# Kernel tuning notes

Hardware: AMD Instinct MI355X
Metric: run time of the kernel (lower is better)

The kernel has to match this reference:

```python
import jax, jax.numpy as jnp
import numpy as np

N, E, H, D, F_IN = 50000, 400000, 2, 128, 5
EPS = 1e-5  # BatchNorm eps

def _bn(x, gamma, beta, rm, rv):
    # eval-mode BatchNorm1d using running stats
    return (x - rm) * jax.lax.rsqrt(rv + EPS) * gamma + beta

def setup_inputs() -> dict:
    key = jax.random.key(0)
    ks = jax.random.split(key, 24)
    r = lambda i, shape, s=1.0: jax.random.normal(ks[i], shape, jnp.float32) * s
    u = lambda i, shape: jax.random.uniform(ks[i], shape, jnp.float32)
    return {
        "h": r(0, (N, F_IN)),
        "edge_index": jax.random.randint(ks[1], (2, E), 0, N),
        "edge_weight": r(2, (E, 1)),
        # BatchNorm1d(5)
        "gamma1": 1.0 + r(3, (F_IN,), 0.1), "beta1": r(4, (F_IN,), 0.1),
        "rm1": r(5, (F_IN,), 0.1), "rv1": 0.5 + u(6, (F_IN,)),
        # GATv2Conv params (lin_l, lin_r with bias; lin_edge no bias; att; out bias)
        "Wl": r(7, (F_IN, H * D), 0.2), "bl": r(8, (H * D,), 0.1),
        "Wr": r(9, (F_IN, H * D), 0.2), "br": r(10, (H * D,), 0.1),
        "We": r(11, (1, H * D), 0.2),
        "att": r(12, (H, D), 0.2),
        "bias_gat": r(13, (D,), 0.1),
        # fc1 + BatchNorm1d(128)
        "W1": r(14, (D, D), 0.08), "b1": r(15, (D,), 0.1),
        "gamma2": 1.0 + r(16, (D,), 0.1), "beta2": r(17, (D,), 0.1),
        "rm2": r(18, (D,), 0.1), "rv2": 0.5 + u(19, (D,)),
        # fc2
        "W2": r(20, (D, F_IN), 0.08), "b2": r(21, (F_IN,), 0.1),
    }

def reference(h, edge_index, edge_weight, gamma1, beta1, rm1, rv1,
              Wl, bl, Wr, br, We, att, bias_gat,
              W1, b1, gamma2, beta2, rm2, rv2, W2, b2):
    src, dst = edge_index[0], edge_index[1]
    h = _bn(h, gamma1, beta1, rm1, rv1)
    xl = (h @ Wl + bl).reshape(N, H, D)   # source transform (messages)
    xr = (h @ Wr + br).reshape(N, H, D)   # destination transform
    e = (edge_weight @ We).reshape(E, H, D)
    # GATv2: score = att . leaky_relu(x_j + x_i + edge_emb), slope 0.2
    z = jax.nn.leaky_relu(xl[src] + xr[dst] + e, 0.2)          # [E,H,D]
    logits = jnp.einsum('ehd,hd->eh', z, att)                   # [E,H]
    # segment softmax over edges sharing a destination node
    mx = jax.ops.segment_max(logits, dst, num_segments=N)       # [N,H]
    ex = jnp.exp(logits - mx[dst])
    den = jax.ops.segment_sum(ex, dst, num_segments=N)
    alpha = ex / (den[dst] + 1e-16)                             # [E,H]
    msg = xl[src] * alpha[:, :, None]                           # [E,H,D]
    ssum = jax.ops.segment_sum(msg, dst, num_segments=N)        # [N,H,D]
    cnt = jax.ops.segment_sum(jnp.ones((E,), jnp.float32), dst, num_segments=N)
    out = ssum / jnp.maximum(cnt, 1.0)[:, None, None]           # aggr='mean'
    out = out.mean(axis=1) + bias_gat                           # concat=False -> head mean
    out = out @ W1 + b1
    out = _bn(out, gamma2, beta2, rm2, rv2)
    out = jax.nn.leaky_relu(out, 0.01)
    # dropout is identity in eval mode
    out = out @ W2 + b2                                         # [N,5]
    return out
```

## Files before the change

kernel.cpp:

```cpp
#include <hip/hip_runtime.h>

#define N_NODES 50000
#define N_EDGES 400000
#define F_INP 5
#define HD 256
#define BN_EPS 1e-5f

typedef short v8s __attribute__((ext_vector_type(8)));
typedef float v4f __attribute__((ext_vector_type(4)));
typedef unsigned v4u __attribute__((ext_vector_type(4)));

#define OFF_HBN  0
#define OFF_ACC  400000
#define OFF_BPK  1200000
#define OFF_WF   1202048
#define OFF_W2P  1204096

__device__ __forceinline__ unsigned short f2bf(float f) {
    unsigned u = __float_as_uint(f);
    return (unsigned short)((u + 0x7FFFu + ((u >> 16) & 1u)) >> 16);
}
__device__ __forceinline__ unsigned pk2(float a, float b) {
    return (unsigned)f2bf(a) | ((unsigned)f2bf(b) << 16);
}

__device__ __forceinline__ float wcat(int k, int c, const float* Wl, const float* Wr,
                                      const float* We, const float* bl, const float* br) {
    if (k < 5)   return Wl[k * HD + c];
    if (k < 10)  return Wr[(k - 5) * HD + c];
    if (k == 10) return We[c];
    return bl[c] + br[c];
}

__global__ void k_prep(const float* __restrict__ h, const float* __restrict__ g1,
                       const float* __restrict__ be1, const float* __restrict__ rm1,
                       const float* __restrict__ rv1,
                       const float* __restrict__ Wl, const float* __restrict__ bl,
                       const float* __restrict__ Wr, const float* __restrict__ br,
                       const float* __restrict__ We, const float* __restrict__ att,
                       float* __restrict__ hbn8, float* __restrict__ acc,
                       unsigned* __restrict__ Bpk) {
    int i = blockIdx.x * blockDim.x + threadIdx.x;
    if (i < N_NODES * 16) acc[i] = 0.f;
    if (i < N_NODES * 8) {
        int f = i & 7, n = i >> 3;
        float v = 0.f;
        if (f < F_INP) {
            float x = h[n * F_INP + f];
            v = (x - rm1[f]) * rsqrtf(rv1[f] + BN_EPS) * g1[f] + be1[f];
        }
        hbn8[i] = v;
    }
    if (i < 1024) {
        int t = i >> 6, l = i & 63;
        int g = l >> 4, c = t * 16 + (l & 15);
        unsigned d0 = 0, d1 = 0;
        if (g < 3) {
            int kb = 4 * g;
            d0 = pk2(wcat(kb + 0, c, Wl, Wr, We, bl, br),
                     wcat(kb + 1, c, Wl, Wr, We, bl, br));
            d1 = pk2(wcat(kb + 2, c, Wl, Wr, We, bl, br),
                     wcat(kb + 3, c, Wl, Wr, We, bl, br));
        }
        Bpk[(t * 64 + l) * 2 + 0] = d0;
        Bpk[(t * 64 + l) * 2 + 1] = d1;
    }
}

__global__ void k_pack2(const float* __restrict__ Wl, const float* __restrict__ bl,
                        const float* __restrict__ bias_gat,
                        const float* __restrict__ W1, const float* __restrict__ b1,
                        const float* __restrict__ g2, const float* __restrict__ be2,
                        const float* __restrict__ rm2, const float* __restrict__ rv2,
                        const float* __restrict__ W2,
                        float* __restrict__ Wf, float* __restrict__ W2p) {
    int k = blockIdx.x;
    int c = threadIdx.x;
    const float* base = (k == 0) ? bl
                      : (k == 1) ? bl + 128
                      : (k < 7)  ? Wl + (k - 2) * HD
                      : (k < 12) ? Wl + (k - 7) * HD + 128
                                 : bias_gat;
    float sum = 0.f;
#pragma unroll 8
    for (int d = 0; d < 128; ++d) sum += base[d] * W1[d * 128 + c];
    if (k == 12) sum += b1[c];
    Wf[c * 16 + k] = sum;
    if (k == 0) {
        float sc = g2[c] * rsqrtf(rv2[c] + BN_EPS);
        Wf[c * 16 + 13] = sc;
        Wf[c * 16 + 14] = be2[c] - rm2[c] * sc;
        Wf[c * 16 + 15] = 0.f;
#pragma unroll
        for (int f = 0; f < 8; ++f)
            W2p[c * 8 + f] = (f < 5) ? W2[c * 5 + f] : 0.f;
    }
}

__launch_bounds__(256)
__global__ void k_edge(const float* __restrict__ hbn8, const int* __restrict__ ei,
                       const float* __restrict__ ew, const unsigned* __restrict__ Bpk,
                       const float* __restrict__ att, float* __restrict__ acc) {
    int lane = threadIdx.x & 63;
    int wv = threadIdx.x >> 6;
    int g = lane >> 4, e16 = lane & 15;

    v8s B[16];
    float AT[16];
#pragma unroll
    for (int t = 0; t < 16; ++t) {
        unsigned d0 = Bpk[(t * 64 + lane) * 2 + 0];
        unsigned d1 = Bpk[(t * 64 + lane) * 2 + 1];
        v4u u = {d0, d1, 0u, 0u};
        B[t] = __builtin_bit_cast(v8s, u);
        AT[t] = att[t * 16 + e16];
    }

    int wid = blockIdx.x * 4 + wv;
    int nw = gridDim.x * 4;
    const int NT = N_EDGES / 16;

    int q13 = lane / 13;
    int j13 = lane - q13 * 13;
    bool sc_act = lane < 52;
    int kk = (j13 < 6) ? j13 - 1 : j13 - 7;
    int kc = min(max(kk, 0), 4);

    float x0 = 0, x1 = 0, x2 = 0, x3 = 0, x4 = 0,
          x5 = 0, x6 = 0, x7 = 0, x8 = 0, x9 = 0, x10 = 0;
    int dst_reg = 0;
    if (wid < NT && lane < 16) {
        int e = wid * 16 + lane;
        int src = ei[e];
        dst_reg = ei[N_EDGES + e];
        x10 = ew[e];
        float4 s4 = *(const float4*)&hbn8[src * 8];
        x0 = s4.x; x1 = s4.y; x2 = s4.z; x3 = s4.w;
        x4 = hbn8[src * 8 + 4];
        float4 d4 = *(const float4*)&hbn8[dst_reg * 8];
        x5 = d4.x; x6 = d4.y; x7 = d4.z; x8 = d4.w;
        x9 = hbn8[dst_reg * 8 + 4];
    }

    for (int tile = wid; tile < NT; tile += nw) {
        float b0 = __shfl(x0, e16), b1 = __shfl(x1, e16), b2 = __shfl(x2, e16),
              b3 = __shfl(x3, e16), b4 = __shfl(x4, e16), b5 = __shfl(x5, e16),
              b6 = __shfl(x6, e16), b7 = __shfl(x7, e16), b8 = __shfl(x8, e16),
              b9 = __shfl(x9, e16), b10 = __shfl(x10, e16);
        int dst_b = __shfl(dst_reg, e16);

        float a0 = (g == 0) ? b0 : (g == 1) ? b4 : b8;
        float a1 = (g == 0) ? b1 : (g == 1) ? b5 : b9;
        float a2 = (g == 0) ? b2 : (g == 1) ? b6 : b10;
        float a3 = (g == 0) ? b3 : (g == 1) ? b7 : 1.0f;
        unsigned ua0 = (g < 3) ? pk2(a0, a1) : 0u;
        unsigned ua1 = (g < 3) ? pk2(a2, a3) : 0u;
        v4u uav = {ua0, ua1, 0u, 0u};
        v8s A = __builtin_bit_cast(v8s, uav);

        int tn = tile + nw;
        if (tn < NT && lane < 16) {
            int e = tn * 16 + lane;
            int src = ei[e];
            dst_reg = ei[N_EDGES + e];
            x10 = ew[e];
            float4 s4 = *(const float4*)&hbn8[src * 8];
            x0 = s4.x; x1 = s4.y; x2 = s4.z; x3 = s4.w;
            x4 = hbn8[src * 8 + 4];
            float4 d4 = *(const float4*)&hbn8[dst_reg * 8];
            x5 = d4.x; x6 = d4.y; x7 = d4.z; x8 = d4.w;
            x9 = hbn8[dst_reg * 8 + 4];
        }

        float p00 = 0.f, p01 = 0.f, p02 = 0.f, p03 = 0.f;
        float p10 = 0.f, p11 = 0.f, p12 = 0.f, p13v = 0.f;
        v4f zero = {0.f, 0.f, 0.f, 0.f};
#pragma unroll
        for (int t = 0; t < 8; ++t) {
            v4f c = __builtin_amdgcn_mfma_f32_16x16x32_bf16(A, B[t], zero, 0, 0, 0);
            p00 += AT[t] * fmaf(0.66666667f, fabsf(c[0]), c[0]);
            p01 += AT[t] * fmaf(0.66666667f, fabsf(c[1]), c[1]);
            p02 += AT[t] * fmaf(0.66666667f, fabsf(c[2]), c[2]);
            p03 += AT[t] * fmaf(0.66666667f, fabsf(c[3]), c[3]);
        }
#pragma unroll
        for (int t = 8; t < 16; ++t) {
            v4f c = __builtin_amdgcn_mfma_f32_16x16x32_bf16(A, B[t], zero, 0, 0, 0);
            p10 += AT[t] * fmaf(0.66666667f, fabsf(c[0]), c[0]);
            p11 += AT[t] * fmaf(0.66666667f, fabsf(c[1]), c[1]);
            p12 += AT[t] * fmaf(0.66666667f, fabsf(c[2]), c[2]);
            p13v += AT[t] * fmaf(0.66666667f, fabsf(c[3]), c[3]);
        }
#pragma unroll
        for (int m = 1; m <= 8; m <<= 1) {
            p00 += __shfl_xor(p00, m); p01 += __shfl_xor(p01, m);
            p02 += __shfl_xor(p02, m); p03 += __shfl_xor(p03, m);
            p10 += __shfl_xor(p10, m); p11 += __shfl_xor(p11, m);
            p12 += __shfl_xor(p12, m); p13v += __shfl_xor(p13v, m);
        }
        float e00 = __expf(0.6f * p00), e01 = __expf(0.6f * p01);
        float e02 = __expf(0.6f * p02), e03 = __expf(0.6f * p03);
        float e10 = __expf(0.6f * p10), e11 = __expf(0.6f * p11);
        float e12 = __expf(0.6f * p12), e13 = __expf(0.6f * p13v);
        float tA0 = (lane & 1) ? e01 : e00;
        float tA1 = (lane & 1) ? e03 : e02;
        float exA = (lane & 2) ? tA1 : tA0;
        float tB0 = (lane & 1) ? e11 : e10;
        float tB1 = (lane & 1) ? e13 : e12;
        float exB = (lane & 2) ? tB1 : tB0;

        if (sc_act) {
#pragma unroll
            for (int it = 0; it < 4; ++it) {
                int es = it * 4 + q13;
                float h0 = __shfl(b0, es), h1 = __shfl(b1, es), h2 = __shfl(b2, es),
                      h3 = __shfl(b3, es), h4 = __shfl(b4, es);
                int de = __shfl(dst_b, es);
                float xh0 = __shfl(exA, it * 16 + q13);
                float xh1 = __shfl(exB, it * 16 + q13);
                float hsel = h0;
                hsel = (kc == 1) ? h1 : hsel;
                hsel = (kc == 2) ? h2 : hsel;
                hsel = (kc == 3) ? h3 : hsel;
                hsel = (kc == 4) ? h4 : hsel;
                float base = (j13 < 6) ? xh0 : xh1;
                float v = base * hsel;
                v = (j13 == 0) ? xh0 : v;
                v = (j13 == 6) ? xh1 : v;
                v = (j13 == 12) ? 1.0f : v;
                atomicAdd(&acc[de * 16 + j13], v);
            }
        }
    }
}

__launch_bounds__(256)
__global__ void k_mlp(const float* __restrict__ acc, const float* __restrict__ Wf,
                      const float* __restrict__ W2p, const float* __restrict__ b2,
                      float* __restrict__ out) {
    int n = blockIdx.x * blockDim.x + threadIdx.x;
    if (n >= N_NODES) return;
    const float* ar = acc + (size_t)n * 16;
    float4 A0 = *(const float4*)(ar + 0);
    float4 A1 = *(const float4*)(ar + 4);
    float4 A2 = *(const float4*)(ar + 8);
    float cnt = ar[12];
    float r0 = 1.f / (A0.x + 1e-16f);
    float r1 = 1.f / (A1.z + 1e-16f);
    float scale = 0.5f / fmaxf(cnt, 1.f);
    float s0 = scale * r0, s1 = scale * r1;
    float m0 = A0.x * s0, m1 = A1.z * s1;
    float m2 = A0.y * s0, m3 = A0.z * s0, m4 = A0.w * s0, m5 = A1.x * s0, m6 = A1.y * s0;
    float m7 = A1.w * s1, m8 = A2.x * s1, m9 = A2.y * s1, m10 = A2.z * s1, m11 = A2.w * s1;

    float o0 = 0.f, o1 = 0.f, o2 = 0.f, o3 = 0.f, o4 = 0.f;
#pragma unroll 4
    for (int c = 0; c < 128; ++c) {
        const float* wr = &Wf[c * 16];
        float a = wr[12];
        a += m0 * wr[0] + m1 * wr[1] + m2 * wr[2] + m3 * wr[3];
        a += m4 * wr[4] + m5 * wr[5] + m6 * wr[6] + m7 * wr[7];
        a += m8 * wr[8] + m9 * wr[9] + m10 * wr[10] + m11 * wr[11];
        a = fmaf(a, wr[13], wr[14]);
        a = fmaxf(a, 0.01f * a);
        const float* w2 = &W2p[c * 8];
        o0 = fmaf(a, w2[0], o0);
        o1 = fmaf(a, w2[1], o1);
        o2 = fmaf(a, w2[2], o2);
        o3 = fmaf(a, w2[3], o3);
        o4 = fmaf(a, w2[4], o4);
    }
    float* op = out + (size_t)n * 5;
    op[0] = o0 + b2[0];
    op[1] = o1 + b2[1];
    op[2] = o2 + b2[2];
    op[3] = o3 + b2[3];
    op[4] = o4 + b2[4];
}

extern "C" void kernel_launch(void* const* d_in, const int* in_sizes, int n_in,
                              void* d_out, int out_size, void* d_ws, size_t ws_size,
                              hipStream_t stream) {
    const float* h    = (const float*)d_in[0];
    const int*   ei   = (const int*)d_in[1];
    const float* ew   = (const float*)d_in[2];
    const float* g1   = (const float*)d_in[3];
    const float* be1  = (const float*)d_in[4];
    const float* rm1  = (const float*)d_in[5];
    const float* rv1  = (const float*)d_in[6];
    const float* Wl   = (const float*)d_in[7];
    const float* bl   = (const float*)d_in[8];
    const float* Wr   = (const float*)d_in[9];
    const float* br   = (const float*)d_in[10];
    const float* We   = (const float*)d_in[11];
    const float* att  = (const float*)d_in[12];
    const float* bias_gat = (const float*)d_in[13];
    const float* W1   = (const float*)d_in[14];
    const float* b1   = (const float*)d_in[15];
    const float* g2   = (const float*)d_in[16];
    const float* be2  = (const float*)d_in[17];
    const float* rm2  = (const float*)d_in[18];
    const float* rv2  = (const float*)d_in[19];
    const float* W2   = (const float*)d_in[20];
    const float* b2   = (const float*)d_in[21];

    float* ws  = (float*)d_ws;
    float* hbn = ws + OFF_HBN;
    float* acc = ws + OFF_ACC;
    unsigned* Bpk = (unsigned*)(ws + OFF_BPK);
    float* Wf  = ws + OFF_WF;
    float* W2p = ws + OFF_W2P;

    k_prep<<<(N_NODES * 16 + 255) / 256, 256, 0, stream>>>(
        h, g1, be1, rm1, rv1, Wl, bl, Wr, br, We, att, hbn, acc, Bpk);
    k_pack2<<<13, 128, 0, stream>>>(Wl, bl, bias_gat, W1, b1, g2, be2, rm2, rv2, W2,
                                    Wf, W2p);
    k_edge<<<1024, 256, 0, stream>>>(hbn, ei, ew, Bpk, att, acc);
    k_mlp<<<(N_NODES + 255) / 256, 256, 0, stream>>>(acc, Wf, W2p, b2, (float*)d_out);
}
```

Baseline: 87.45 us.

## Merge pack kernel into prep and split edge kernel into two variants

Folds the weight-folding pack kernel into the prep kernel as extra blocks, which removes one launch. The edge pass is split across two kernels, each covering half the edge tiles. The first half uses a new variant with direct loads and DPP row-rotate reductions in place of shuffles, and the second keeps the prefetching shuffle version. This adds a launch and duplicates the weight-fragment setup per kernel, in exchange for trying a different reduction and load scheme on half the work.

```diff
diff --git a/kernel.cpp b/kernel.cpp
--- a/kernel.cpp
+++ b/kernel.cpp
@@ -15,6 +15,13 @@
 #define OFF_BPK  1200000
 #define OFF_WF   1202048
 #define OFF_W2P  1204096
+
+#define PREP_BLOCKS 3125
+#define NT_ALL   25000
+#define NT_HALF  12500
+
+#define DPP_ROR_F(x, n) \
+    __int_as_float(__builtin_amdgcn_update_dpp(0, __float_as_int(x), 0x120 | (n), 0xF, 0xF, false))
 
 __device__ __forceinline__ unsigned short f2bf(float f) {
     unsigned u = __float_as_uint(f);
@@ -38,44 +45,45 @@
                        const float* __restrict__ Wl, const float* __restrict__ bl,
                        const float* __restrict__ Wr, const float* __restrict__ br,
                        const float* __restrict__ We, const float* __restrict__ att,
+                       const float* __restrict__ bias_gat,
+                       const float* __restrict__ W1, const float* __restrict__ b1,
+                       const float* __restrict__ g2, const float* __restrict__ be2,
+                       const float* __restrict__ rm2, const float* __restrict__ rv2,
+                       const float* __restrict__ W2,
                        float* __restrict__ hbn8, float* __restrict__ acc,
-                       unsigned* __restrict__ Bpk) {
-    int i = blockIdx.x * blockDim.x + threadIdx.x;
-    if (i < N_NODES * 16) acc[i] = 0.f;
-    if (i < N_NODES * 8) {
-        int f = i & 7, n = i >> 3;
-        float v = 0.f;
-        if (f < F_INP) {
-            float x = h[n * F_INP + f];
-            v = (x - rm1[f]) * rsqrtf(rv1[f] + BN_EPS) * g1[f] + be1[f];
-        }
-        hbn8[i] = v;
-    }
-    if (i < 1024) {
-        int t = i >> 6, l = i & 63;
-        int g = l >> 4, c = t * 16 + (l & 15);
-        unsigned d0 = 0, d1 = 0;
-        if (g < 3) {
-            int kb = 4 * g;
-            d0 = pk2(wcat(kb + 0, c, Wl, Wr, We, bl, br),
-                     wcat(kb + 1, c, Wl, Wr, We, bl, br));
-            d1 = pk2(wcat(kb + 2, c, Wl, Wr, We, bl, br),
-                     wcat(kb + 3, c, Wl, Wr, We, bl, br));
-        }
-        Bpk[(t * 64 + l) * 2 + 0] = d0;
-        Bpk[(t * 64 + l) * 2 + 1] = d1;
-    }
-}
-
-__global__ void k_pack2(const float* __restrict__ Wl, const float* __restrict__ bl,
-                        const float* __restrict__ bias_gat,
-                        const float* __restrict__ W1, const float* __restrict__ b1,
-                        const float* __restrict__ g2, const float* __restrict__ be2,
-                        const float* __restrict__ rm2, const float* __restrict__ rv2,
-                        const float* __restrict__ W2,
-                        float* __restrict__ Wf, float* __restrict__ W2p) {
-    int k = blockIdx.x;
+                       unsigned* __restrict__ Bpk,
+                       float* __restrict__ Wf, float* __restrict__ W2p) {
+    if (blockIdx.x < PREP_BLOCKS) {
+        int i = blockIdx.x * blockDim.x + threadIdx.x;
+        if (i < N_NODES * 16) acc[i] = 0.f;
+        if (i < N_NODES * 8) {
+            int f = i & 7, n = i >> 3;
+            float v = 0.f;
+            if (f < F_INP) {
+                float x = h[n * F_INP + f];
+                v = (x - rm1[f]) * rsqrtf(rv1[f] + BN_EPS) * g1[f] + be1[f];
+            }
+            hbn8[i] = v;
+        }
+        if (i < 1024) {
+            int t = i >> 6, l = i & 63;
+            int g = l >> 4, c = t * 16 + (l & 15);
+            unsigned d0 = 0, d1 = 0;
+            if (g < 3) {
+                int kb = 4 * g;
+                d0 = pk2(wcat(kb + 0, c, Wl, Wr, We, bl, br),
+                         wcat(kb + 1, c, Wl, Wr, We, bl, br));
+                d1 = pk2(wcat(kb + 2, c, Wl, Wr, We, bl, br),
+                         wcat(kb + 3, c, Wl, Wr, We, bl, br));
+            }
+            Bpk[(t * 64 + l) * 2 + 0] = d0;
+            Bpk[(t * 64 + l) * 2 + 1] = d1;
+        }
+        return;
+    }
+    int k = blockIdx.x - PREP_BLOCKS;
     int c = threadIdx.x;
+    if (c >= 128) return;
     const float* base = (k == 0) ? bl
                       : (k == 1) ? bl + 128
                       : (k < 7)  ? Wl + (k - 2) * HD
@@ -98,9 +106,9 @@
 }
 
 __launch_bounds__(256)
-__global__ void k_edge(const float* __restrict__ hbn8, const int* __restrict__ ei,
-                       const float* __restrict__ ew, const unsigned* __restrict__ Bpk,
-                       const float* __restrict__ att, float* __restrict__ acc) {
+__global__ void k_edge_a(const float* __restrict__ hbn8, const int* __restrict__ ei,
+                         const float* __restrict__ ew, const unsigned* __restrict__ Bpk,
+                         const float* __restrict__ att, float* __restrict__ acc) {
     int lane = threadIdx.x & 63;
     int wv = threadIdx.x >> 6;
     int g = lane >> 4, e16 = lane & 15;
@@ -109,16 +117,120 @@
     float AT[16];
 #pragma unroll
     for (int t = 0; t < 16; ++t) {
-        unsigned d0 = Bpk[(t * 64 + lane) * 2 + 0];
-        unsigned d1 = Bpk[(t * 64 + lane) * 2 + 1];
-        v4u u = {d0, d1, 0u, 0u};
+        uint2 d = *(const uint2*)&Bpk[(t * 64 + lane) * 2];
+        v4u u = {d.x, d.y, 0u, 0u};
         B[t] = __builtin_bit_cast(v8s, u);
         AT[t] = att[t * 16 + e16];
     }
 
     int wid = blockIdx.x * 4 + wv;
     int nw = gridDim.x * 4;
-    const int NT = N_EDGES / 16;
+
+    int j16 = e16;
+    bool sact = j16 < 13;
+    int kk = (j16 < 6) ? j16 - 1 : j16 - 7;
+    int kc = min(max(kk, 0), 4);
+
+    for (int tile = wid; tile < NT_HALF; tile += nw) {
+        int e = tile * 16 + e16;
+        int src = ei[e];
+        int dst = ei[N_EDGES + e];
+        float w = ew[e];
+        float4 s4 = *(const float4*)&hbn8[src * 8];
+        float hs4 = hbn8[src * 8 + 4];
+        float4 d4 = *(const float4*)&hbn8[dst * 8];
+        float hd4 = hbn8[dst * 8 + 4];
+
+        float a0 = (g == 0) ? s4.x : (g == 1) ? hs4  : d4.w;
+        float a1 = (g == 0) ? s4.y : (g == 1) ? d4.x : hd4;
+        float a2 = (g == 0) ? s4.z : (g == 1) ? d4.y : w;
+        float a3 = (g == 0) ? s4.w : (g == 1) ? d4.z : 1.0f;
+        unsigned ua0 = (g < 3) ? pk2(a0, a1) : 0u;
+        unsigned ua1 = (g < 3) ? pk2(a2, a3) : 0u;
+        v4u uav = {ua0, ua1, 0u, 0u};
+        v8s A = __builtin_bit_cast(v8s, uav);
+
+        float p00 = 0.f, p01 = 0.f, p02 = 0.f, p03 = 0.f;
+        float p10 = 0.f, p11 = 0.f, p12 = 0.f, p13v = 0.f;
+        v4f zero = {0.f, 0.f, 0.f, 0.f};
+#pragma unroll
+        for (int t = 0; t < 8; ++t) {
+            v4f c = __builtin_amdgcn_mfma_f32_16x16x32_bf16(A, B[t], zero, 0, 0, 0);
+            p00 += AT[t] * fmaf(0.66666667f, fabsf(c[0]), c[0]);
+            p01 += AT[t] * fmaf(0.66666667f, fabsf(c[1]), c[1]);
+            p02 += AT[t] * fmaf(0.66666667f, fabsf(c[2]), c[2]);
+            p03 += AT[t] * fmaf(0.66666667f, fabsf(c[3]), c[3]);
+        }
+#pragma unroll
+        for (int t = 8; t < 16; ++t) {
+            v4f c = __builtin_amdgcn_mfma_f32_16x16x32_bf16(A, B[t], zero, 0, 0, 0);
+            p10 += AT[t] * fmaf(0.66666667f, fabsf(c[0]), c[0]);
+            p11 += AT[t] * fmaf(0.66666667f, fabsf(c[1]), c[1]);
+            p12 += AT[t] * fmaf(0.66666667f, fabsf(c[2]), c[2]);
+            p13v += AT[t] * fmaf(0.66666667f, fabsf(c[3]), c[3]);
+        }
+        p00 += DPP_ROR_F(p00, 1); p01 += DPP_ROR_F(p01, 1);
+        p02 += DPP_ROR_F(p02, 1); p03 += DPP_ROR_F(p03, 1);
+        p10 += DPP_ROR_F(p10, 1); p11 += DPP_ROR_F(p11, 1);
+        p12 += DPP_ROR_F(p12, 1); p13v += DPP_ROR_F(p13v, 1);
+        p00 += DPP_ROR_F(p00, 2); p01 += DPP_ROR_F(p01, 2);
+        p02 += DPP_ROR_F(p02, 2); p03 += DPP_ROR_F(p03, 2);
+        p10 += DPP_ROR_F(p10, 2); p11 += DPP_ROR_F(p11, 2);
+        p12 += DPP_ROR_F(p12, 2); p13v += DPP_ROR_F(p13v, 2);
+        p00 += DPP_ROR_F(p00, 4); p01 += DPP_ROR_F(p01, 4);
+        p02 += DPP_ROR_F(p02, 4); p03 += DPP_ROR_F(p03, 4);
+        p10 += DPP_ROR_F(p10, 4); p11 += DPP_ROR_F(p11, 4);
+        p12 += DPP_ROR_F(p12, 4); p13v += DPP_ROR_F(p13v, 4);
+        p00 += DPP_ROR_F(p00, 8); p01 += DPP_ROR_F(p01, 8);
+        p02 += DPP_ROR_F(p02, 8); p03 += DPP_ROR_F(p03, 8);
+        p10 += DPP_ROR_F(p10, 8); p11 += DPP_ROR_F(p11, 8);
+        p12 += DPP_ROR_F(p12, 8); p13v += DPP_ROR_F(p13v, 8);
+
+        float e00 = __expf(0.6f * p00), e01 = __expf(0.6f * p01);
+        float e02 = __expf(0.6f * p02), e03 = __expf(0.6f * p03);
+        float e10 = __expf(0.6f * p10), e11 = __expf(0.6f * p11);
+        float e12 = __expf(0.6f * p12), e13 = __expf(0.6f * p13v);
+
+        if (sact) {
+#pragma unroll
+            for (int it = 0; it < 4; ++it) {
+                int eg = tile * 16 + 4 * g + it;
+                int srcg = ei[eg];
+                int deg = ei[N_EDGES + eg];
+                float hsel = hbn8[srcg * 8 + kc];
+                float ex0 = (it == 0) ? e00 : (it == 1) ? e01 : (it == 2) ? e02 : e03;
+                float ex1 = (it == 0) ? e10 : (it == 1) ? e11 : (it == 2) ? e12 : e13;
+                float base = (j16 < 6) ? ex0 : ex1;
+                float v = base * hsel;
+                v = (j16 == 0) ? ex0 : v;
+                v = (j16 == 6) ? ex1 : v;
+                v = (j16 == 12) ? 1.0f : v;
+                atomicAdd(&acc[deg * 16 + j16], v);
+            }
+        }
+    }
+}
+
+__launch_bounds__(256)
+__global__ void k_edge_b(const float* __restrict__ hbn8, const int* __restrict__ ei,
+                         const float* __restrict__ ew, const unsigned* __restrict__ Bpk,
+                         const float* __restrict__ att, float* __restrict__ acc) {
+    int lane = threadIdx.x & 63;
+    int wv = threadIdx.x >> 6;
+    int g = lane >> 4, e16 = lane & 15;
+
+    v8s B[16];
+    float AT[16];
+#pragma unroll
+    for (int t = 0; t < 16; ++t) {
+        uint2 d = *(const uint2*)&Bpk[(t * 64 + lane) * 2];
+        v4u u = {d.x, d.y, 0u, 0u};
+        B[t] = __builtin_bit_cast(v8s, u);
+        AT[t] = att[t * 16 + e16];
+    }
+
+    int wid = blockIdx.x * 4 + wv;
+    int nw = gridDim.x * 4;
 
     int q13 = lane / 13;
     int j13 = lane - q13 * 13;
@@ -129,8 +241,9 @@
     float x0 = 0, x1 = 0, x2 = 0, x3 = 0, x4 = 0,
           x5 = 0, x6 = 0, x7 = 0, x8 = 0, x9 = 0, x10 = 0;
     int dst_reg = 0;
-    if (wid < NT && lane < 16) {
-        int e = wid * 16 + lane;
+    int tile0 = NT_HALF + wid;
+    if (tile0 < NT_ALL && lane < 16) {
+        int e = tile0 * 16 + lane;
         int src = ei[e];
         dst_reg = ei[N_EDGES + e];
         x10 = ew[e];
@@ -142,7 +255,7 @@
         x9 = hbn8[dst_reg * 8 + 4];
     }
 
-    for (int tile = wid; tile < NT; tile += nw) {
+    for (int tile = tile0; tile < NT_ALL; tile += nw) {
         float b0 = __shfl(x0, e16), b1 = __shfl(x1, e16), b2 = __shfl(x2, e16),
               b3 = __shfl(x3, e16), b4 = __shfl(x4, e16), b5 = __shfl(x5, e16),
               b6 = __shfl(x6, e16), b7 = __shfl(x7, e16), b8 = __shfl(x8, e16),
@@ -159,7 +272,7 @@
         v8s A = __builtin_bit_cast(v8s, uav);
 
         int tn = tile + nw;
-        if (tn < NT && lane < 16) {
+        if (tn < NT_ALL && lane < 16) {
             int e = tn * 16 + lane;
             int src = ei[e];
             dst_reg = ei[N_EDGES + e];
@@ -311,10 +424,10 @@
     float* Wf  = ws + OFF_WF;
     float* W2p = ws + OFF_W2P;
 
-    k_prep<<<(N_NODES * 16 + 255) / 256, 256, 0, stream>>>(
-        h, g1, be1, rm1, rv1, Wl, bl, Wr, br, We, att, hbn, acc, Bpk);
-    k_pack2<<<13, 128, 0, stream>>>(Wl, bl, bias_gat, W1, b1, g2, be2, rm2, rv2, W2,
-                                    Wf, W2p);
-    k_edge<<<1024, 256, 0, stream>>>(hbn, ei, ew, Bpk, att, acc);
+    k_prep<<<PREP_BLOCKS + 13, 256, 0, stream>>>(
+        h, g1, be1, rm1, rv1, Wl, bl, Wr, br, We, att, bias_gat,
+        W1, b1, g2, be2, rm2, rv2, W2, hbn, acc, Bpk, Wf, W2p);
+    k_edge_a<<<640, 256, 0, stream>>>(hbn, ei, ew, Bpk, att, acc);
+    k_edge_b<<<640, 256, 0, stream>>>(hbn, ei, ew, Bpk, att, acc);
     k_mlp<<<(N_NODES + 255) / 256, 256, 0, stream>>>(acc, Wf, W2p, b2, (float*)d_out);
 }
```

After: 89.54 us (median of 2 runs). +2.4%, slower.
